# Kernel optimization log

Measured on AMD Instinct MI355X. Metric: run time of the kernel, lower is better.

Reference implementation:

```python
import jax, jax.numpy as jnp
import numpy as np

B, S, D, H = 2, 2048, 1024, 16
HD = D // H  # 64

def _make_freqs():
    # flux-style rotation matrices: [1,1,S,HD//2,2,2]
    theta = 10000.0
    inv = 1.0 / (theta ** (np.arange(0, HD, 2, dtype=np.float32) / HD))  # [HD//2]
    pos = np.arange(S, dtype=np.float32)
    ang = pos[:, None] * inv[None, :]  # [S, HD//2]
    cos, sin = np.cos(ang), np.sin(ang)
    rot = np.stack([np.stack([cos, -sin], -1), np.stack([sin, cos], -1)], -2)  # [S,HD//2,2,2]
    return jnp.asarray(rot[None, None], dtype=jnp.float32)

def setup_inputs() -> dict:
    key = jax.random.key(0)
    ks = jax.random.split(key, 9)
    sc = 1.0 / np.sqrt(D)
    return {
        "x": jax.random.normal(ks[0], (B, S, D), jnp.float32),
        "freqs": _make_freqs(),
        "Wq": jax.random.normal(ks[1], (D, D), jnp.float32) * sc,
        "bq": jax.random.normal(ks[2], (D,), jnp.float32) * 0.01,
        "Wk": jax.random.normal(ks[3], (D, D), jnp.float32) * sc,
        "bk": jax.random.normal(ks[4], (D,), jnp.float32) * 0.01,
        "Wv": jax.random.normal(ks[5], (D, D), jnp.float32) * sc,
        "bv": jax.random.normal(ks[6], (D,), jnp.float32) * 0.01,
        "Wo": jax.random.normal(ks[7], (D, D), jnp.float32) * sc,
        "bo": jax.random.normal(ks[8], (D,), jnp.float32) * 0.01,
    }

def _apply_rope(xq, xk, freqs):
    # xq/xk: [B,H,S,HD]; freqs: [1,1,S,HD//2,2,2]
    def rot(t):
        t_ = t.reshape(*t.shape[:-1], -1, 1, 2)  # [B,H,S,HD//2,1,2]
        out = freqs[..., 0] * t_[..., 0] + freqs[..., 1] * t_[..., 1]  # [B,H,S,HD//2,2]
        return out.reshape(t.shape).astype(t.dtype)
    return rot(xq), rot(xk)

def reference(x, freqs, Wq, bq, Wk, bk, Wv, bv, Wo, bo):
    b, s, _ = x.shape
    # QKV projections (torch Linear: x @ W.T + b)
    q = (x @ Wq.T + bq).reshape(b, s, H, HD).transpose(0, 2, 1, 3)  # [B,H,S,HD]
    k = (x @ Wk.T + bk).reshape(b, s, H, HD).transpose(0, 2, 1, 3)
    v = (x @ Wv.T + bv).reshape(b, s, H, HD).transpose(0, 2, 1, 3)
    q, k = _apply_rope(q, k, freqs)
    # scaled dot product attention, no mask, no dropout
    scale = 1.0 / jnp.sqrt(jnp.asarray(HD, x.dtype))
    scores = jnp.einsum("bhqd,bhkd->bhqk", q, k) * scale
    attn = jax.nn.softmax(scores, axis=-1)
    o = jnp.einsum("bhqk,bhkd->bhqd", attn, v)  # [B,H,S,HD]
    o = o.transpose(0, 2, 1, 3).reshape(b, s, D)
    return o @ Wo.T + bo
```

## Files before the change

### kernel.cpp

```cpp
#include <hip/hip_runtime.h>
#include <cmath>

#define B_ 2
#define S_ 2048
#define D_ 1024
#define H_ 16
#define HD_ 64
#define M_ 4096

typedef __attribute__((ext_vector_type(8))) short short8;
typedef __attribute__((ext_vector_type(4))) short short4v;
typedef __attribute__((ext_vector_type(4))) float f32x4;

__device__ __forceinline__ short f2bf(float x) {
    unsigned u = __builtin_bit_cast(unsigned, x);
    u += 0x7fffu + ((u >> 16) & 1u);
    return (short)(u >> 16);
}

__device__ __forceinline__ void gload_lds16(const short* g, short* l) {
    __builtin_amdgcn_global_load_lds(
        (const __attribute__((address_space(1))) unsigned int*)g,
        (__attribute__((address_space(3))) unsigned int*)l, 16, 0, 0);
}

__global__ __launch_bounds__(256) void cast_all_kernel(
    const float* __restrict__ x,  const float* __restrict__ Wq,
    const float* __restrict__ Wk, const float* __restrict__ Wv,
    const float* __restrict__ Wo,
    short* __restrict__ xb, short* __restrict__ Wqkvb, short* __restrict__ Wob)
{
    const size_t i = (size_t)blockIdx.x * 256 + threadIdx.x;
    const float* src; short* dst; size_t off;
    if (i < 1048576)      { src = x;  dst = xb;              off = i; }
    else if (i < 1310720) { src = Wq; dst = Wqkvb;           off = i - 1048576; }
    else if (i < 1572864) { src = Wk; dst = Wqkvb + 1048576; off = i - 1310720; }
    else if (i < 1835008) { src = Wv; dst = Wqkvb + 2097152; off = i - 1572864; }
    else                  { src = Wo; dst = Wob;             off = i - 1835008; }
    float4 v = ((const float4*)src)[off];
    short4v o = { f2bf(v.x), f2bf(v.y), f2bf(v.z), f2bf(v.w) };
    ((short4v*)dst)[off] = o;
}

template<int MODE, int TM, int TN>
__global__ __launch_bounds__(256) void gemm_mfma(
    const short* __restrict__ A, const short* __restrict__ Bw,
    const float* __restrict__ b0p, const float* __restrict__ b1p, const float* __restrict__ b2p,
    const float* __restrict__ freqs,
    void* __restrict__ out0, void* __restrict__ out1, void* __restrict__ out2)
{
    constexpr int RT = TM / 32, CT = TN / 32;
    __shared__ __align__(16) short As[2][TM*32];
    __shared__ __align__(16) short Bs[2][TN*32];
    const int t = threadIdx.x;
    const int w = t >> 6;
    const int lane = t & 63;
    const int qd = lane >> 4, l = lane & 15;
    const int n0 = blockIdx.x * TN, m0 = blockIdx.y * TM;
    const int wr = (w >> 1) * (TM/2), wc = (w & 1) * (TN/2);
    const int srow = lane >> 2;
    const int scol = (lane & 3) * 8;

    #define STAGE(buf, k0)                                                         \
        do {                                                                       \
            _Pragma("unroll")                                                      \
            for (int j = 0; j < TM/64; ++j) {                                      \
                const int rr = (j*4 + w) * 16;                                     \
                gload_lds16(A  + (size_t)(m0 + rr + srow)*1024 + (k0) + scol,      \
                            &As[buf][rr*32]);                                      \
            }                                                                      \
            _Pragma("unroll")                                                      \
            for (int j = 0; j < TN/64; ++j) {                                      \
                const int rr = (j*4 + w) * 16;                                     \
                gload_lds16(Bw + (size_t)(n0 + rr + srow)*1024 + (k0) + scol,      \
                            &Bs[buf][rr*32]);                                      \
            }                                                                      \
        } while (0)

    f32x4 acc[RT][CT] = {};
    STAGE(0, 0);

    for (int k0 = 0; k0 < 1024; k0 += 32) {
        const int cur = (k0 >> 5) & 1;
        __syncthreads();
        if (k0 + 32 < 1024) STAGE(cur ^ 1, k0 + 32);
        short8 af[RT], bf[CT];
        #pragma unroll
        for (int rt = 0; rt < RT; ++rt)
            af[rt] = *(const short8*)&As[cur][(wr + rt*16 + l)*32 + qd*8];
        #pragma unroll
        for (int ct = 0; ct < CT; ++ct)
            bf[ct] = *(const short8*)&Bs[cur][(wc + ct*16 + l)*32 + qd*8];
        #pragma unroll
        for (int rt = 0; rt < RT; ++rt)
            #pragma unroll
            for (int ct = 0; ct < CT; ++ct)
                acc[rt][ct] = __builtin_amdgcn_mfma_f32_16x16x32_bf16(af[rt], bf[ct], acc[rt][ct], 0, 0, 0);
    }
    #undef STAGE

    if (MODE == 0) {
        float* out = (float*)out0;
        #pragma unroll
        for (int rt = 0; rt < RT; ++rt)
            #pragma unroll
            for (int ct = 0; ct < CT; ++ct) {
                const int n = n0 + wc + ct*16 + l;
                const float bias = b0p[n];
                #pragma unroll
                for (int r = 0; r < 4; ++r) {
                    const int m = m0 + wr + rt*16 + qd*4 + r;
                    out[(size_t)m*1024 + n] = acc[rt][ct][r] + bias;
                }
            }
    } else {
        const int sel = n0 >> 10;
        const int nb = n0 & 1023;
        const float* bias = (sel == 0) ? b0p : (sel == 1) ? b1p : b2p;
        if (sel < 2) {
            short* outg = (short*)((sel == 0) ? out0 : out1);
            #pragma unroll
            for (int rt = 0; rt < RT; ++rt)
                #pragma unroll
                for (int ct = 0; ct < CT; ++ct) {
                    const int d = nb + wc + ct*16 + l;
                    const float bsv = bias[d];
                    const int h = d >> 6, hd = d & 63;
                    #pragma unroll
                    for (int r = 0; r < 4; ++r) {
                        const int m = m0 + wr + rt*16 + qd*4 + r;
                        const int bb = m >> 11, s = m & 2047;
                        float val = acc[rt][ct][r] + bsv;
                        float pv = __shfl_xor(val, 1);
                        const float* f = freqs + (size_t)s*128 + (size_t)(hd >> 1)*4;
                        float o = (d & 1) ? (f[2]*pv + f[3]*val) : (f[0]*val + f[1]*pv);
                        outg[((size_t)(bb*16 + h)*2048 + s)*64 + hd] = f2bf(o);
                    }
                }
        } else {
            short* outv = (short*)out2;
            #pragma unroll
            for (int rt = 0; rt < RT; ++rt)
                #pragma unroll
                for (int ct = 0; ct < CT; ++ct) {
                    const int d = nb + wc + ct*16 + l;
                    const float bsv = bias[d];
                    const int h = d >> 6, hd = d & 63;
                    const int m0r = m0 + wr + rt*16 + qd*4;
                    const int bb = m0r >> 11, s0 = m0r & 2047;
                    short4v pk;
                    #pragma unroll
                    for (int r = 0; r < 4; ++r) pk[r] = f2bf(acc[rt][ct][r] + bsv);
                    *(short4v*)&outv[((size_t)(bb*16 + h)*64 + hd)*2048 + s0] = pk;
                }
        }
    }
}

__global__ __launch_bounds__(256) void attn_mfma(
    const short* __restrict__ qg, const short* __restrict__ kg,
    const short* __restrict__ vtg, short* __restrict__ og)
{
    __shared__ __align__(16) short KP[128*136];
    __shared__ __align__(16) short Vt[64*136];

    const int t = threadIdx.x;
    const int w = t >> 6;
    const int lane = t & 63;
    const int qd = lane >> 4, l = lane & 15;
    const int q0 = blockIdx.x * 128;
    const int bh = blockIdx.y;

    short8 qf[2][2];
    const short* qb = qg + ((size_t)bh*2048 + q0 + w*32)*64;
    #pragma unroll
    for (int rt = 0; rt < 2; ++rt)
        #pragma unroll
        for (int kf = 0; kf < 2; ++kf)
            qf[rt][kf] = *(const short8*)&qb[(rt*16 + l)*64 + kf*32 + qd*8];

    f32x4 oacc[2][4] = {};
    float lsum[2] = {};

    const short* kbase = kg  + (size_t)bh*2048*64;
    const short* vbase = vtg + (size_t)bh*64*2048;
    const float SC = 0.125f * 1.44269504088896340736f;

    for (int kt = 0; kt < 16; ++kt) {
        __syncthreads();
        {
            const short* src = kbase + (size_t)(kt*128 + (t>>1))*64 + (t&1)*32;
            short* dst = &KP[(t>>1)*136 + (t&1)*32];
            *(short8*)(dst+0)  = *(const short8*)(src+0);
            *(short8*)(dst+8)  = *(const short8*)(src+8);
            *(short8*)(dst+16) = *(const short8*)(src+16);
            *(short8*)(dst+24) = *(const short8*)(src+24);
        }
        {
            const short* src = vbase + (size_t)(t>>2)*2048 + kt*128 + (t&3)*32;
            short* dst = &Vt[(t>>2)*136 + (t&3)*32];
            *(short8*)(dst+0)  = *(const short8*)(src+0);
            *(short8*)(dst+8)  = *(const short8*)(src+8);
            *(short8*)(dst+16) = *(const short8*)(src+16);
            *(short8*)(dst+24) = *(const short8*)(src+24);
        }
        __syncthreads();

        f32x4 sacc[2][8] = {};
        #pragma unroll
        for (int ct = 0; ct < 8; ++ct) {
            short8 k0f = *(const short8*)&KP[(ct*16 + l)*136 + qd*8];
            short8 k1f = *(const short8*)&KP[(ct*16 + l)*136 + 32 + qd*8];
            #pragma unroll
            for (int rt = 0; rt < 2; ++rt) {
                sacc[rt][ct] = __builtin_amdgcn_mfma_f32_16x16x32_bf16(k0f, qf[rt][0], sacc[rt][ct], 0, 0, 0);
                sacc[rt][ct] = __builtin_amdgcn_mfma_f32_16x16x32_bf16(k1f, qf[rt][1], sacc[rt][ct], 0, 0, 0);
            }
        }
        __syncthreads();

        #pragma unroll
        for (int rt = 0; rt < 2; ++rt)
            #pragma unroll
            for (int ct = 0; ct < 8; ++ct) {
                short4v pk;
                #pragma unroll
                for (int r = 0; r < 4; ++r) {
                    float p = exp2f(sacc[rt][ct][r] * SC);
                    lsum[rt] += p;
                    pk[r] = f2bf(p);
                }
                *(short4v*)&KP[(w*32 + rt*16 + l)*136 + ct*16 + qd*4] = pk;
            }

        #pragma unroll
        for (int kf = 0; kf < 4; ++kf) {
            short8 pa0 = *(const short8*)&KP[(w*32 +  0 + l)*136 + kf*32 + qd*8];
            short8 pa1 = *(const short8*)&KP[(w*32 + 16 + l)*136 + kf*32 + qd*8];
            #pragma unroll
            for (int ht = 0; ht < 4; ++ht) {
                short8 vb = *(const short8*)&Vt[(ht*16 + l)*136 + kf*32 + qd*8];
                oacc[0][ht] = __builtin_amdgcn_mfma_f32_16x16x32_bf16(pa0, vb, oacc[0][ht], 0, 0, 0);
                oacc[1][ht] = __builtin_amdgcn_mfma_f32_16x16x32_bf16(pa1, vb, oacc[1][ht], 0, 0, 0);
            }
        }
    }

    #pragma unroll
    for (int rt = 0; rt < 2; ++rt) {
        lsum[rt] += __shfl_xor(lsum[rt], 16);
        lsum[rt] += __shfl_xor(lsum[rt], 32);
    }
    float inv[2][4];
    #pragma unroll
    for (int rt = 0; rt < 2; ++rt)
        #pragma unroll
        for (int r = 0; r < 4; ++r)
            inv[rt][r] = 1.0f / __shfl(lsum[rt], qd*4 + r);

    const int bb = bh >> 4, h = bh & 15;
    #pragma unroll
    for (int rt = 0; rt < 2; ++rt)
        #pragma unroll
        for (int ht = 0; ht < 4; ++ht)
            #pragma unroll
            for (int r = 0; r < 4; ++r) {
                const int s = q0 + w*32 + rt*16 + qd*4 + r;
                og[((size_t)bb*2048 + s)*1024 + h*64 + ht*16 + l] =
                    f2bf(oacc[rt][ht][r] * inv[rt][r]);
            }
}

extern "C" void kernel_launch(void* const* d_in, const int* in_sizes, int n_in,
                              void* d_out, int out_size, void* d_ws, size_t ws_size,
                              hipStream_t stream)
{
    const float* x  = (const float*)d_in[0];
    const float* fr = (const float*)d_in[1];
    const float* Wq = (const float*)d_in[2];
    const float* bq = (const float*)d_in[3];
    const float* Wk = (const float*)d_in[4];
    const float* bk = (const float*)d_in[5];
    const float* Wv = (const float*)d_in[6];
    const float* bv = (const float*)d_in[7];
    const float* Wo = (const float*)d_in[8];
    const float* bo = (const float*)d_in[9];
    float* out = (float*)d_out;

    short* ws    = (short*)d_ws;
    short* xb    = ws;
    short* Wqkvb = xb    + 4194304;
    short* Wob   = Wqkvb + 3145728;
    short* qg    = Wob   + 1048576;
    short* kg    = qg    + 4194304;
    short* vtg   = kg    + 4194304;
    short* og    = vtg   + 4194304;

    cast_all_kernel<<<8192, 256, 0, stream>>>(x, Wq, Wk, Wv, Wo, xb, Wqkvb, Wob);
    gemm_mfma<1,128,128><<<dim3(24, 32), 256, 0, stream>>>(xb, Wqkvb, bq, bk, bv, fr, qg, kg, vtg);
    attn_mfma<<<dim3(16, 32), 256, 0, stream>>>(qg, kg, vtg, og);
    gemm_mfma<0,64,64><<<dim3(16, 64), 256, 0, stream>>>(og, Wob, bo, nullptr, nullptr, nullptr,
                                                         out, nullptr, nullptr);
}
```

Baseline: 282.3 us.

## Drop GEMM double buffering, shrink attention and QKV tiles, split P buffer

The GEMM loses its double-buffered LDS prefetch and now loads each K-slice synchronously between two barriers. The QKV projection tile goes from 128x128 to 128x64, doubling the grid. Attention now handles 64 query rows per block instead of 128, with one 16-row tile per wave, a separate P buffer in LDS, and a narrower K stride, so one barrier is gone. The aim is more resident blocks and less register/LDS pressure, but it loses the copy/compute overlap in the GEMMs and reloads K/V twice as often in attention.

```diff
diff --git a/kernel.cpp b/kernel.cpp
--- a/kernel.cpp
+++ b/kernel.cpp
@@ -43,15 +43,15 @@
 }
 
 template<int MODE, int TM, int TN>
-__global__ __launch_bounds__(256) void gemm_mfma(
+__global__ __launch_bounds__(256) void gemm_tile(
     const short* __restrict__ A, const short* __restrict__ Bw,
     const float* __restrict__ b0p, const float* __restrict__ b1p, const float* __restrict__ b2p,
     const float* __restrict__ freqs,
     void* __restrict__ out0, void* __restrict__ out1, void* __restrict__ out2)
 {
     constexpr int RT = TM / 32, CT = TN / 32;
-    __shared__ __align__(16) short As[2][TM*32];
-    __shared__ __align__(16) short Bs[2][TN*32];
+    __shared__ __align__(16) short As[TM*32];
+    __shared__ __align__(16) short Bs[TN*32];
     const int t = threadIdx.x;
     const int w = t >> 6;
     const int lane = t & 63;
@@ -61,43 +61,34 @@
     const int srow = lane >> 2;
     const int scol = (lane & 3) * 8;
 
-    #define STAGE(buf, k0)                                                         \
-        do {                                                                       \
-            _Pragma("unroll")                                                      \
-            for (int j = 0; j < TM/64; ++j) {                                      \
-                const int rr = (j*4 + w) * 16;                                     \
-                gload_lds16(A  + (size_t)(m0 + rr + srow)*1024 + (k0) + scol,      \
-                            &As[buf][rr*32]);                                      \
-            }                                                                      \
-            _Pragma("unroll")                                                      \
-            for (int j = 0; j < TN/64; ++j) {                                      \
-                const int rr = (j*4 + w) * 16;                                     \
-                gload_lds16(Bw + (size_t)(n0 + rr + srow)*1024 + (k0) + scol,      \
-                            &Bs[buf][rr*32]);                                      \
-            }                                                                      \
-        } while (0)
-
     f32x4 acc[RT][CT] = {};
-    STAGE(0, 0);
 
     for (int k0 = 0; k0 < 1024; k0 += 32) {
-        const int cur = (k0 >> 5) & 1;
-        __syncthreads();
-        if (k0 + 32 < 1024) STAGE(cur ^ 1, k0 + 32);
+        __syncthreads();
+        #pragma unroll
+        for (int j = 0; j < TM/64; ++j) {
+            const int rr = (j*4 + w) * 16;
+            gload_lds16(A + (size_t)(m0 + rr + srow)*1024 + k0 + scol, &As[rr*32]);
+        }
+        #pragma unroll
+        for (int j = 0; j < TN/64; ++j) {
+            const int rr = (j*4 + w) * 16;
+            gload_lds16(Bw + (size_t)(n0 + rr + srow)*1024 + k0 + scol, &Bs[rr*32]);
+        }
+        __syncthreads();
         short8 af[RT], bf[CT];
         #pragma unroll
         for (int rt = 0; rt < RT; ++rt)
-            af[rt] = *(const short8*)&As[cur][(wr + rt*16 + l)*32 + qd*8];
+            af[rt] = *(const short8*)&As[(wr + rt*16 + l)*32 + qd*8];
         #pragma unroll
         for (int ct = 0; ct < CT; ++ct)
-            bf[ct] = *(const short8*)&Bs[cur][(wc + ct*16 + l)*32 + qd*8];
+            bf[ct] = *(const short8*)&Bs[(wc + ct*16 + l)*32 + qd*8];
         #pragma unroll
         for (int rt = 0; rt < RT; ++rt)
             #pragma unroll
             for (int ct = 0; ct < CT; ++ct)
                 acc[rt][ct] = __builtin_amdgcn_mfma_f32_16x16x32_bf16(af[rt], bf[ct], acc[rt][ct], 0, 0, 0);
     }
-    #undef STAGE
 
     if (MODE == 0) {
         float* out = (float*)out0;
@@ -161,26 +152,25 @@
     const short* __restrict__ qg, const short* __restrict__ kg,
     const short* __restrict__ vtg, short* __restrict__ og)
 {
-    __shared__ __align__(16) short KP[128*136];
+    __shared__ __align__(16) short Kt[128*68];
     __shared__ __align__(16) short Vt[64*136];
+    __shared__ __align__(16) short Ps[64*136];
 
     const int t = threadIdx.x;
     const int w = t >> 6;
     const int lane = t & 63;
     const int qd = lane >> 4, l = lane & 15;
-    const int q0 = blockIdx.x * 128;
+    const int q0 = blockIdx.x * 64;
     const int bh = blockIdx.y;
 
-    short8 qf[2][2];
-    const short* qb = qg + ((size_t)bh*2048 + q0 + w*32)*64;
+    short8 qf[2];
+    const short* qb = qg + ((size_t)bh*2048 + q0 + w*16)*64;
     #pragma unroll
-    for (int rt = 0; rt < 2; ++rt)
-        #pragma unroll
-        for (int kf = 0; kf < 2; ++kf)
-            qf[rt][kf] = *(const short8*)&qb[(rt*16 + l)*64 + kf*32 + qd*8];
-
-    f32x4 oacc[2][4] = {};
-    float lsum[2] = {};
+    for (int kf = 0; kf < 2; ++kf)
+        qf[kf] = *(const short8*)&qb[l*64 + kf*32 + qd*8];
+
+    f32x4 oacc[4] = {};
+    float lsum = 0.f;
 
     const short* kbase = kg  + (size_t)bh*2048*64;
     const short* vbase = vtg + (size_t)bh*64*2048;
@@ -190,7 +180,7 @@
         __syncthreads();
         {
             const short* src = kbase + (size_t)(kt*128 + (t>>1))*64 + (t&1)*32;
-            short* dst = &KP[(t>>1)*136 + (t&1)*32];
+            short* dst = &Kt[(t>>1)*68 + (t&1)*32];
             *(short8*)(dst+0)  = *(const short8*)(src+0);
             *(short8*)(dst+8)  = *(const short8*)(src+8);
             *(short8*)(dst+16) = *(const short8*)(src+16);
@@ -206,69 +196,54 @@
         }
         __syncthreads();
 
-        f32x4 sacc[2][8] = {};
+        f32x4 sacc[8] = {};
         #pragma unroll
         for (int ct = 0; ct < 8; ++ct) {
-            short8 k0f = *(const short8*)&KP[(ct*16 + l)*136 + qd*8];
-            short8 k1f = *(const short8*)&KP[(ct*16 + l)*136 + 32 + qd*8];
-            #pragma unroll
-            for (int rt = 0; rt < 2; ++rt) {
-                sacc[rt][ct] = __builtin_amdgcn_mfma_f32_16x16x32_bf16(k0f, qf[rt][0], sacc[rt][ct], 0, 0, 0);
-                sacc[rt][ct] = __builtin_amdgcn_mfma_f32_16x16x32_bf16(k1f, qf[rt][1], sacc[rt][ct], 0, 0, 0);
+            short8 k0f = *(const short8*)&Kt[(ct*16 + l)*68 + qd*8];
+            short8 k1f = *(const short8*)&Kt[(ct*16 + l)*68 + 32 + qd*8];
+            sacc[ct] = __builtin_amdgcn_mfma_f32_16x16x32_bf16(k0f, qf[0], sacc[ct], 0, 0, 0);
+            sacc[ct] = __builtin_amdgcn_mfma_f32_16x16x32_bf16(k1f, qf[1], sacc[ct], 0, 0, 0);
+        }
+
+        #pragma unroll
+        for (int ct = 0; ct < 8; ++ct) {
+            short4v pk;
+            #pragma unroll
+            for (int r = 0; r < 4; ++r) {
+                float p = exp2f(sacc[ct][r] * SC);
+                lsum += p;
+                pk[r] = f2bf(p);
             }
-        }
-        __syncthreads();
-
-        #pragma unroll
-        for (int rt = 0; rt < 2; ++rt)
-            #pragma unroll
-            for (int ct = 0; ct < 8; ++ct) {
-                short4v pk;
-                #pragma unroll
-                for (int r = 0; r < 4; ++r) {
-                    float p = exp2f(sacc[rt][ct][r] * SC);
-                    lsum[rt] += p;
-                    pk[r] = f2bf(p);
-                }
-                *(short4v*)&KP[(w*32 + rt*16 + l)*136 + ct*16 + qd*4] = pk;
-            }
+            *(short4v*)&Ps[(w*16 + l)*136 + ct*16 + qd*4] = pk;
+        }
 
         #pragma unroll
         for (int kf = 0; kf < 4; ++kf) {
-            short8 pa0 = *(const short8*)&KP[(w*32 +  0 + l)*136 + kf*32 + qd*8];
-            short8 pa1 = *(const short8*)&KP[(w*32 + 16 + l)*136 + kf*32 + qd*8];
+            short8 pa = *(const short8*)&Ps[(w*16 + l)*136 + kf*32 + qd*8];
             #pragma unroll
             for (int ht = 0; ht < 4; ++ht) {
                 short8 vb = *(const short8*)&Vt[(ht*16 + l)*136 + kf*32 + qd*8];
-                oacc[0][ht] = __builtin_amdgcn_mfma_f32_16x16x32_bf16(pa0, vb, oacc[0][ht], 0, 0, 0);
-                oacc[1][ht] = __builtin_amdgcn_mfma_f32_16x16x32_bf16(pa1, vb, oacc[1][ht], 0, 0, 0);
+                oacc[ht] = __builtin_amdgcn_mfma_f32_16x16x32_bf16(pa, vb, oacc[ht], 0, 0, 0);
             }
         }
     }
 
+    lsum += __shfl_xor(lsum, 16);
+    lsum += __shfl_xor(lsum, 32);
+    float inv[4];
     #pragma unroll
-    for (int rt = 0; rt < 2; ++rt) {
-        lsum[rt] += __shfl_xor(lsum[rt], 16);
-        lsum[rt] += __shfl_xor(lsum[rt], 32);
-    }
-    float inv[2][4];
-    #pragma unroll
-    for (int rt = 0; rt < 2; ++rt)
-        #pragma unroll
-        for (int r = 0; r < 4; ++r)
-            inv[rt][r] = 1.0f / __shfl(lsum[rt], qd*4 + r);
+    for (int r = 0; r < 4; ++r)
+        inv[r] = 1.0f / __shfl(lsum, qd*4 + r);
 
     const int bb = bh >> 4, h = bh & 15;
     #pragma unroll
-    for (int rt = 0; rt < 2; ++rt)
-        #pragma unroll
-        for (int ht = 0; ht < 4; ++ht)
-            #pragma unroll
-            for (int r = 0; r < 4; ++r) {
-                const int s = q0 + w*32 + rt*16 + qd*4 + r;
-                og[((size_t)bb*2048 + s)*1024 + h*64 + ht*16 + l] =
-                    f2bf(oacc[rt][ht][r] * inv[rt][r]);
-            }
+    for (int ht = 0; ht < 4; ++ht)
+        #pragma unroll
+        for (int r = 0; r < 4; ++r) {
+            const int s = q0 + w*16 + qd*4 + r;
+            og[((size_t)bb*2048 + s)*1024 + h*64 + ht*16 + l] =
+                f2bf(oacc[ht][r] * inv[r]);
+        }
 }
 
 extern "C" void kernel_launch(void* const* d_in, const int* in_sizes, int n_in,
@@ -297,8 +272,8 @@
     short* og    = vtg   + 4194304;
 
     cast_all_kernel<<<8192, 256, 0, stream>>>(x, Wq, Wk, Wv, Wo, xb, Wqkvb, Wob);
-    gemm_mfma<1,128,128><<<dim3(24, 32), 256, 0, stream>>>(xb, Wqkvb, bq, bk, bv, fr, qg, kg, vtg);
-    attn_mfma<<<dim3(16, 32), 256, 0, stream>>>(qg, kg, vtg, og);
-    gemm_mfma<0,64,64><<<dim3(16, 64), 256, 0, stream>>>(og, Wob, bo, nullptr, nullptr, nullptr,
+    gemm_tile<1,128,64><<<dim3(48, 32), 256, 0, stream>>>(xb, Wqkvb, bq, bk, bv, fr, qg, kg, vtg);
+    attn_mfma<<<dim3(32, 32), 256, 0, stream>>>(qg, kg, vtg, og);
+    gemm_tile<0,64,64><<<dim3(16, 64), 256, 0, stream>>>(og, Wob, bo, nullptr, nullptr, nullptr,
                                                          out, nullptr, nullptr);
 }
```

Measured after the change: 289.1 us. 1.02x slower.
